# Optimization experiments

Hardware: AMD Instinct MI355X
Metric: run time of the kernel (lower is better)

The kernel has to match this reference:

```python
import jax, jax.numpy as jnp
import numpy as np

B, LC, LQ, H = 64, 1024, 128, 512
NEG = -1e30


def setup_inputs() -> dict:
    key = jax.random.key(0)
    ks = jax.random.split(key, 12)
    s = 1.0 / np.sqrt(H)
    return {
        "c": jax.random.normal(ks[0], (B, LC, H), jnp.float32),
        "q": jax.random.normal(ks[1], (B, LQ, H), jnp.float32),
        "c_mask": jax.random.randint(ks[2], (B, LC), 0, 2, jnp.int32),
        "q_mask": jax.random.randint(ks[3], (B, LQ), 0, 2, jnp.int32),
        "c_weight": jax.random.normal(ks[4], (H, 1), jnp.float32) * s,
        "q_weight": jax.random.normal(ks[5], (H, 1), jnp.float32) * s,
        "cq_weight": jax.random.normal(ks[6], (1, 1, H), jnp.float32) * s,
        "bias": jnp.zeros((1,), jnp.float32),
        "W1": jax.random.normal(ks[7], (H, H), jnp.float32) * s,
        "b1": jnp.zeros((H,), jnp.float32),
        "W2": jax.random.normal(ks[8], (H, H), jnp.float32) * s,
        "b2": jnp.zeros((H,), jnp.float32),
    }


def reference(c, q, c_mask, q_mask, c_weight, q_weight, cq_weight, bias, W1, b1, W2, b2):
    # --- trilinear similarity (BiDAF eq. 1, memory-efficient form) ---
    s0 = c @ c_weight                                   # [B, LC, 1]
    s1 = jnp.swapaxes(q @ q_weight, 1, 2)               # [B, 1, LQ]
    s2 = jnp.einsum('bch,bqh->bcq', c * cq_weight, q)   # [B, LC, LQ]
    sim = s0 + s1 + s2 + bias

    qm = (q_mask != 0)[:, None, :]   # [B, 1, LQ]
    cm = (c_mask != 0)[:, :, None]   # [B, LC, 1]

    # dual masked softmax (dropout is identity in eval mode)
    s1s = jax.nn.softmax(jnp.where(qm, sim, NEG), axis=2)  # c2q weights
    s2s = jax.nn.softmax(jnp.where(cm, sim, NEG), axis=1)  # q2c weights

    a = s1s @ q                                            # [B, LC, H]
    b = jnp.einsum('bcq,bkq->bck', s1s, s2s) @ c           # [B, LC, H]

    # co-attention branch: qprime = relu(lin2(relu(lin1(q))))
    qp = jax.nn.relu(jax.nn.relu(q @ W1 + b1) @ W2 + b2)   # [B, LQ, H]
    scoat = jnp.einsum('bch,bqh->bcq', c, qp)              # [B, LC, LQ]
    sc1 = jax.nn.softmax(jnp.where(qm, scoat, NEG), axis=2)
    sc2 = jax.nn.softmax(jnp.where(cm, scoat, NEG), axis=1)
    acoat = sc1 @ qp                                       # [B, LC, H]
    bcoat = jnp.einsum('bcq,bch->bqh', sc2, c)             # [B, LQ, H]
    scoat3 = sc1 @ bcoat                                   # [B, LC, H]

    return jnp.concatenate([c, a, c * a, c * b, scoat3, acoat], axis=2)  # [B, LC, 6H]
```

## Files before the change

### kernel.cpp

```cpp
#include <hip/hip_runtime.h>
#include <cstdint>
#include <cstddef>

typedef short  bf16x8 __attribute__((ext_vector_type(8)));
typedef float  f32x4  __attribute__((ext_vector_type(4)));

#define NEGV (-1e30f)
#define LDT 40

__device__ __forceinline__ short f2bf(float x){
    union { float f; unsigned u; } v; v.f = x;
    return (short)((v.u + 0x7fffu + ((v.u >> 16) & 1u)) >> 16);
}
__device__ __forceinline__ float bf2f(short h){
    union { float f; unsigned u; } v; v.u = ((unsigned)(unsigned short)h) << 16; return v.f;
}

__global__ __launch_bounds__(256)
void k_prep_w(const float* __restrict__ W1, const float* __restrict__ W2,
              short* __restrict__ W1Th, short* __restrict__ W1Tl,
              short* __restrict__ W2Th, short* __restrict__ W2Tl)
{
    int idx = blockIdx.x * 256 + threadIdx.x;
    int w = idx >> 18;
    int e = idx & ((1 << 18) - 1);
    int n = e & 511, k = e >> 9;
    const float* W = w ? W2 : W1;
    float x = W[k * 512 + n];
    short hi = f2bf(x);
    short lo = f2bf(x - bf2f(hi));
    size_t o = (size_t)n * 512 + k;
    if (w) { W2Th[o] = hi; W2Tl[o] = lo; } else { W1Th[o] = hi; W1Tl[o] = lo; }
}

__global__ __launch_bounds__(256)
void k_transq(const float* __restrict__ q, short* __restrict__ qT)
{
    __shared__ short TT[128 * 136];
    const int t = threadIdx.x;
    const int b = (int)(blockIdx.x >> 2), h0 = (int)(blockIdx.x & 3) * 128;
    #pragma unroll
    for (int it = 0; it < 16; it++) {
        int idx = it * 256 + t;
        int m = idx >> 5, c4 = (idx & 31) * 4;
        float4 v = *(const float4*)(q + ((size_t)b * 128 + m) * 512 + h0 + c4);
        TT[(c4 + 0) * 136 + m] = f2bf(v.x);
        TT[(c4 + 1) * 136 + m] = f2bf(v.y);
        TT[(c4 + 2) * 136 + m] = f2bf(v.z);
        TT[(c4 + 3) * 136 + m] = f2bf(v.w);
    }
    __syncthreads();
    const int h = t >> 1, half = t & 1;
    short* dst = qT + ((size_t)b * 512 + h0 + h) * 128 + half * 64;
    #pragma unroll
    for (int j = 0; j < 8; j++)
        *(bf16x8*)(dst + j * 8) = *(const bf16x8*)&TT[h * 136 + half * 64 + j * 8];
}

template<bool WT>
__global__ __launch_bounds__(256)
void k_linear(const float* __restrict__ X, const short* __restrict__ WTh,
              const short* __restrict__ WTl, const float* __restrict__ bias,
              float* __restrict__ Y, short* __restrict__ YT)
{
    __shared__ short SMEM[4 * 128 * LDT];
    short* Ah = SMEM;
    short* Al = SMEM + 128 * LDT;
    short* Bh = SMEM + 2 * 128 * LDT;
    short* Bl = SMEM + 3 * 128 * LDT;
    const int t = threadIdx.x;
    const int m0 = (int)(blockIdx.x >> 2) * 128;
    const int n0 = (int)(blockIdx.x & 3) * 128;
    const int lane = t & 63;
    const int wr = (t >> 7) & 1, wc = (t >> 6) & 1;
    const int fr = lane & 15, fg = lane >> 4;
    const int srow = t >> 1, sk = (t & 1) * 16;

    f32x4 acc[4][4] = {};

    for (int k0 = 0; k0 < 512; k0 += 32) {
        __syncthreads();
        {
            const float* src = X + (size_t)(m0 + srow) * 512 + k0 + sk;
            float4 f[4];
            #pragma unroll
            for (int i = 0; i < 4; i++) f[i] = ((const float4*)src)[i];
            const float* fv = (const float*)f;
            short hi[16], lo[16];
            #pragma unroll
            for (int j = 0; j < 16; j++) {
                float x = fv[j];
                short h = f2bf(x);
                hi[j] = h; lo[j] = f2bf(x - bf2f(h));
            }
            #pragma unroll
            for (int j = 0; j < 2; j++) {
                *(bf16x8*)&Ah[srow * LDT + sk + j * 8] = *(bf16x8*)&hi[j * 8];
                *(bf16x8*)&Al[srow * LDT + sk + j * 8] = *(bf16x8*)&lo[j * 8];
            }
        }
        {
            const short* sh = WTh + (size_t)(n0 + srow) * 512 + k0 + sk;
            const short* sl = WTl + (size_t)(n0 + srow) * 512 + k0 + sk;
            #pragma unroll
            for (int j = 0; j < 2; j++) {
                *(bf16x8*)&Bh[srow * LDT + sk + j * 8] = ((const bf16x8*)sh)[j];
                *(bf16x8*)&Bl[srow * LDT + sk + j * 8] = ((const bf16x8*)sl)[j];
            }
        }
        __syncthreads();
        bf16x8 a_h[4], a_l[4], b_h[4], b_l[4];
        #pragma unroll
        for (int i = 0; i < 4; i++) {
            int ar = (wr * 64 + i * 16 + fr) * LDT + fg * 8;
            int br = (wc * 64 + i * 16 + fr) * LDT + fg * 8;
            a_h[i] = *(const bf16x8*)&Ah[ar];
            a_l[i] = *(const bf16x8*)&Al[ar];
            b_h[i] = *(const bf16x8*)&Bh[br];
            b_l[i] = *(const bf16x8*)&Bl[br];
        }
        #pragma unroll
        for (int mi = 0; mi < 4; mi++)
        #pragma unroll
        for (int ni = 0; ni < 4; ni++) {
            acc[mi][ni] = __builtin_amdgcn_mfma_f32_16x16x32_bf16(a_h[mi], b_h[ni], acc[mi][ni], 0, 0, 0);
            acc[mi][ni] = __builtin_amdgcn_mfma_f32_16x16x32_bf16(a_h[mi], b_l[ni], acc[mi][ni], 0, 0, 0);
            acc[mi][ni] = __builtin_amdgcn_mfma_f32_16x16x32_bf16(a_l[mi], b_h[ni], acc[mi][ni], 0, 0, 0);
        }
    }
    float bv[4];
    #pragma unroll
    for (int ni = 0; ni < 4; ni++) bv[ni] = bias[n0 + wc * 64 + ni * 16 + fr];
    #pragma unroll
    for (int mi = 0; mi < 4; mi++)
    #pragma unroll
    for (int r = 0; r < 4; r++) {
        int row = m0 + wr * 64 + mi * 16 + fg * 4 + r;
        #pragma unroll
        for (int ni = 0; ni < 4; ni++) {
            float v = fmaxf(acc[mi][ni][r] + bv[ni], 0.f);
            Y[(size_t)row * 512 + n0 + wc * 64 + ni * 16 + fr] = v;
        }
    }
    if (WT) {
        __syncthreads();
        short* TT = SMEM;
        #pragma unroll
        for (int mi = 0; mi < 4; mi++)
        #pragma unroll
        for (int r = 0; r < 4; r++) {
            int ml = wr * 64 + mi * 16 + fg * 4 + r;
            #pragma unroll
            for (int ni = 0; ni < 4; ni++) {
                int nl = wc * 64 + ni * 16 + fr;
                TT[nl * 136 + ml] = f2bf(fmaxf(acc[mi][ni][r] + bv[ni], 0.f));
            }
        }
        __syncthreads();
        const int n = t >> 1, half = t & 1;
        short* dst = YT + ((size_t)(m0 >> 7) * 512 + n0 + n) * 128 + half * 64;
        #pragma unroll
        for (int j = 0; j < 8; j++)
            *(bf16x8*)(dst + j * 8) = *(const bf16x8*)&TT[n * 136 + half * 64 + j * 8];
    }
}

template<bool SPLIT, bool AMUL, bool ADDS>
__global__ __launch_bounds__(256)
void k_att_gemm(const float* __restrict__ Cc, const float* __restrict__ Qq,
                const float* __restrict__ cqw, const float* __restrict__ cwv,
                const float* __restrict__ qwv, const float* __restrict__ biasp,
                const int* __restrict__ qmask, const int* __restrict__ cmask,
                float* __restrict__ Sout, float2* __restrict__ rowst,
                float2* __restrict__ colpart)
{
    __shared__ short Ah[128 * LDT], Bh[128 * LDT];
    __shared__ short Al[SPLIT ? 128 * LDT : 8], Bl[SPLIT ? 128 * LDT : 8];
    __shared__ float cqs[AMUL ? 512 : 8];
    __shared__ float cws[ADDS ? 512 : 8], qws[ADDS ? 512 : 8];
    __shared__ float red[2][128];
    __shared__ float mrowL[128], cmaxL[128];
    __shared__ float s0red[ADDS ? 128 : 1][2], s1red[ADDS ? 128 : 1][2];
    __shared__ float s0arr[ADDS ? 128 : 1], s1arr[ADDS ? 128 : 1];
    __shared__ int qmsL[128], cmsL[128];

    const int t = threadIdx.x;
    const int b  = (int)(blockIdx.x >> 3);
    const int ch = (int)(blockIdx.x & 7);
    const int m0 = ch * 128;
    const int lane = t & 63;
    const int wr = (t >> 7) & 1, wc = (t >> 6) & 1;
    const int fr = lane & 15, fg = lane >> 4;
    const int srow = t >> 1, sk = (t & 1) * 16;

    if (AMUL) { cqs[t] = cqw[t]; cqs[t + 256] = cqw[t + 256]; }
    if (ADDS) {
        cws[t] = cwv[t]; cws[t + 256] = cwv[t + 256];
        qws[t] = qwv[t]; qws[t + 256] = qwv[t + 256];
    }
    if (t < 128) { qmsL[t] = qmask[b * 128 + t]; cmsL[t] = cmask[b * 1024 + m0 + t]; }

    float s0part = 0.f, s1part = 0.f;
    f32x4 acc[4][4] = {};

    for (int k0 = 0; k0 < 512; k0 += 32) {
        __syncthreads();
        {
            const float* src = Cc + ((size_t)b * 1024 + m0 + srow) * 512 + k0 + sk;
            float4 f[4];
            #pragma unroll
            for (int i = 0; i < 4; i++) f[i] = ((const float4*)src)[i];
            const float* fv = (const float*)f;
            short hi[16], lo[16];
            #pragma unroll
            for (int j = 0; j < 16; j++) {
                float raw = fv[j];
                if (ADDS) s0part += raw * cws[k0 + sk + j];
                float x = raw;
                if (AMUL) x *= cqs[k0 + sk + j];
                short h = f2bf(x);
                hi[j] = h;
                if (SPLIT) lo[j] = f2bf(x - bf2f(h));
            }
            #pragma unroll
            for (int j = 0; j < 2; j++) {
                *(bf16x8*)&Ah[srow * LDT + sk + j * 8] = *(bf16x8*)&hi[j * 8];
                if (SPLIT) *(bf16x8*)&Al[srow * LDT + sk + j * 8] = *(bf16x8*)&lo[j * 8];
            }
        }
        {
            const float* src = Qq + ((size_t)b * 128 + srow) * 512 + k0 + sk;
            float4 f[4];
            #pragma unroll
            for (int i = 0; i < 4; i++) f[i] = ((const float4*)src)[i];
            const float* fv = (const float*)f;
            short hi[16], lo[16];
            #pragma unroll
            for (int j = 0; j < 16; j++) {
                float x = fv[j];
                if (ADDS) s1part += x * qws[k0 + sk + j];
                short h = f2bf(x);
                hi[j] = h;
                if (SPLIT) lo[j] = f2bf(x - bf2f(h));
            }
            #pragma unroll
            for (int j = 0; j < 2; j++) {
                *(bf16x8*)&Bh[srow * LDT + sk + j * 8] = *(bf16x8*)&hi[j * 8];
                if (SPLIT) *(bf16x8*)&Bl[srow * LDT + sk + j * 8] = *(bf16x8*)&lo[j * 8];
            }
        }
        __syncthreads();
        bf16x8 a_h[4], b_h[4], a_l[4], b_l[4];
        #pragma unroll
        for (int i = 0; i < 4; i++) {
            int ar = (wr * 64 + i * 16 + fr) * LDT + fg * 8;
            int br = (wc * 64 + i * 16 + fr) * LDT + fg * 8;
            a_h[i] = *(const bf16x8*)&Ah[ar];
            b_h[i] = *(const bf16x8*)&Bh[br];
            if (SPLIT) { a_l[i] = *(const bf16x8*)&Al[ar]; b_l[i] = *(const bf16x8*)&Bl[br]; }
        }
        #pragma unroll
        for (int mi = 0; mi < 4; mi++)
        #pragma unroll
        for (int ni = 0; ni < 4; ni++) {
            acc[mi][ni] = __builtin_amdgcn_mfma_f32_16x16x32_bf16(a_h[mi], b_h[ni], acc[mi][ni], 0, 0, 0);
            if (SPLIT) {
                acc[mi][ni] = __builtin_amdgcn_mfma_f32_16x16x32_bf16(a_h[mi], b_l[ni], acc[mi][ni], 0, 0, 0);
                acc[mi][ni] = __builtin_amdgcn_mfma_f32_16x16x32_bf16(a_l[mi], b_h[ni], acc[mi][ni], 0, 0, 0);
            }
        }
    }

    if (ADDS) { s0red[srow][t & 1] = s0part; s1red[srow][t & 1] = s1part; }
    __syncthreads();
    if (ADDS && t < 128) {
        s0arr[t] = s0red[t][0] + s0red[t][1];
        s1arr[t] = s1red[t][0] + s1red[t][1];
    }
    if (ADDS) __syncthreads();

    if (ADDS) {
        float b0 = biasp[0];
        #pragma unroll
        for (int mi = 0; mi < 4; mi++)
        #pragma unroll
        for (int r = 0; r < 4; r++) {
            float s0r = s0arr[wr * 64 + mi * 16 + fg * 4 + r] + b0;
            #pragma unroll
            for (int ni = 0; ni < 4; ni++)
                acc[mi][ni][r] += s0r + s1arr[wc * 64 + ni * 16 + fr];
        }
    }
    #pragma unroll
    for (int mi = 0; mi < 4; mi++)
    #pragma unroll
    for (int r = 0; r < 4; r++) {
        int row = m0 + wr * 64 + mi * 16 + fg * 4 + r;
        #pragma unroll
        for (int ni = 0; ni < 4; ni++)
            Sout[((size_t)b * 1024 + row) * 128 + wc * 64 + ni * 16 + fr] = acc[mi][ni][r];
    }

    bool qmv[4];
    #pragma unroll
    for (int ni = 0; ni < 4; ni++) qmv[ni] = qmsL[wc * 64 + ni * 16 + fr] != 0;
    bool cmb[4][4];
    #pragma unroll
    for (int mi = 0; mi < 4; mi++)
    #pragma unroll
    for (int r = 0; r < 4; r++) cmb[mi][r] = cmsL[wr * 64 + mi * 16 + fg * 4 + r] != 0;

    float rmax[4][4];
    #pragma unroll
    for (int mi = 0; mi < 4; mi++)
    #pragma unroll
    for (int r = 0; r < 4; r++) {
        float m = NEGV;
        #pragma unroll
        for (int ni = 0; ni < 4; ni++) if (qmv[ni]) m = fmaxf(m, acc[mi][ni][r]);
        #pragma unroll
        for (int off = 1; off < 16; off <<= 1) m = fmaxf(m, __shfl_xor(m, off));
        rmax[mi][r] = m;
    }
    if (fr == 0) {
        #pragma unroll
        for (int mi = 0; mi < 4; mi++)
        #pragma unroll
        for (int r = 0; r < 4; r++) red[wc][wr * 64 + mi * 16 + fg * 4 + r] = rmax[mi][r];
    }
    __syncthreads();
    if (t < 128) mrowL[t] = fmaxf(red[0][t], red[1][t]);
    __syncthreads();
    #pragma unroll
    for (int mi = 0; mi < 4; mi++)
    #pragma unroll
    for (int r = 0; r < 4; r++) {
        float mr = mrowL[wr * 64 + mi * 16 + fg * 4 + r];
        float s = 0.f;
        #pragma unroll
        for (int ni = 0; ni < 4; ni++) if (qmv[ni]) s += __expf(acc[mi][ni][r] - mr);
        #pragma unroll
        for (int off = 1; off < 16; off <<= 1) s += __shfl_xor(s, off);
        if (fr == 0) red[wc][wr * 64 + mi * 16 + fg * 4 + r] = s;
    }
    __syncthreads();
    if (t < 128) rowst[(size_t)b * 1024 + m0 + t] = make_float2(mrowL[t], red[0][t] + red[1][t]);
    __syncthreads();
    float cpart[4];
    #pragma unroll
    for (int ni = 0; ni < 4; ni++) {
        float m = NEGV;
        #pragma unroll
        for (int mi = 0; mi < 4; mi++)
        #pragma unroll
        for (int r = 0; r < 4; r++) if (cmb[mi][r]) m = fmaxf(m, acc[mi][ni][r]);
        m = fmaxf(m, __shfl_xor(m, 16));
        m = fmaxf(m, __shfl_xor(m, 32));
        cpart[ni] = m;
    }
    if (fg == 0) {
        #pragma unroll
        for (int ni = 0; ni < 4; ni++) red[wr][wc * 64 + ni * 16 + fr] = cpart[ni];
    }
    __syncthreads();
    if (t < 128) cmaxL[t] = fmaxf(red[0][t], red[1][t]);
    __syncthreads();
    #pragma unroll
    for (int ni = 0; ni < 4; ni++) {
        float cm = cmaxL[wc * 64 + ni * 16 + fr];
        float s = 0.f;
        #pragma unroll
        for (int mi = 0; mi < 4; mi++)
        #pragma unroll
        for (int r = 0; r < 4; r++) if (cmb[mi][r]) s += __expf(acc[mi][ni][r] - cm);
        s += __shfl_xor(s, 16);
        s += __shfl_xor(s, 32);
        cpart[ni] = s;
    }
    __syncthreads();
    if (fg == 0) {
        #pragma unroll
        for (int ni = 0; ni < 4; ni++) red[wr][wc * 64 + ni * 16 + fr] = cpart[ni];
    }
    __syncthreads();
    if (t < 128) colpart[((size_t)b * 8 + ch) * 128 + t] = make_float2(cmaxL[t], red[0][t] + red[1][t]);
}

__global__ __launch_bounds__(512)
void k_emit(const float* __restrict__ S, const int* __restrict__ qmask,
            const int* __restrict__ cmask, const float2* __restrict__ rowst,
            const float2* __restrict__ colpart, short* __restrict__ Pr,
            short* __restrict__ PcT)
{
    __shared__ float2 colfinL[128];
    const int t = threadIdx.x;
    const int b = (int)(blockIdx.x >> 3), ch = (int)(blockIdx.x & 7);
    const int r0 = ch * 128;
    if (t < 128) {
        float M = NEGV;
        #pragma unroll
        for (int c2 = 0; c2 < 8; c2++) M = fmaxf(M, colpart[((size_t)b * 8 + c2) * 128 + t].x);
        float Ss = 0.f;
        #pragma unroll
        for (int c2 = 0; c2 < 8; c2++) {
            float2 p = colpart[((size_t)b * 8 + c2) * 128 + t];
            Ss += p.y * __expf(p.x - M);
        }
        colfinL[t] = make_float2(M, Ss);
    }
    __syncthreads();
    {
        const int q = t & 127, rg = t >> 7;
        const bool qm = qmask[b * 128 + q] != 0;
        #pragma unroll 8
        for (int i = 0; i < 32; i++) {
            int r = r0 + rg * 32 + i;
            size_t idx = ((size_t)b * 1024 + r) * 128 + q;
            float v = S[idx];
            float2 rs = rowst[(size_t)b * 1024 + r];
            float o = qm ? __expf(v - rs.x) / rs.y : 0.f;
            Pr[idx] = f2bf(o);
        }
    }
    {
        const int q2 = t >> 2, ig = t & 3;
        float2 cs = colfinL[q2];
        float inv = 1.f / cs.y;
        short buf[32];
        #pragma unroll
        for (int i = 0; i < 32; i++) {
            int r = r0 + ig * 32 + i;
            bool cm = cmask[b * 1024 + r] != 0;
            float v = S[((size_t)b * 1024 + r) * 128 + q2];
            buf[i] = f2bf(cm ? __expf(v - cs.x) * inv : 0.f);
        }
        short* dst = PcT + ((size_t)b * 128 + q2) * 1024 + r0 + ig * 32;
        #pragma unroll
        for (int j = 0; j < 4; j++) *(bf16x8*)(dst + j * 8) = *(bf16x8*)&buf[j * 8];
    }
}

__global__ __launch_bounds__(256)
void k_kgemm2(const short* __restrict__ A1, const short* __restrict__ A2,
              const float* __restrict__ Cc, short* __restrict__ Y1T,
              short* __restrict__ Y2T)
{
    __shared__ short Bs[128 * LDT];
    __shared__ short TT[128 * 136];
    const int t = threadIdx.x;
    const int b = (int)(blockIdx.x >> 2);
    const int n0 = (int)(blockIdx.x & 3) * 128;
    const int lane = t & 63;
    const int wr = (t >> 7) & 1, wc = (t >> 6) & 1;
    const int fr = lane & 15, fg = lane >> 4;
    const int n4 = (t & 31) * 4, kk4 = (t >> 5) * 4;
    f32x4 acc1[4][4] = {}, acc2[4][4] = {};
    for (int k0 = 0; k0 < 1024; k0 += 32) {
        __syncthreads();
        {
            const float* bsrc = Cc + ((size_t)b * 1024 + k0 + kk4) * 512 + n0 + n4;
            float4 r0_ = *(const float4*)(bsrc);
            float4 r1_ = *(const float4*)(bsrc + 512);
            float4 r2_ = *(const float4*)(bsrc + 1024);
            float4 r3_ = *(const float4*)(bsrc + 1536);
            const float* p0 = (const float*)&r0_;
            const float* p1 = (const float*)&r1_;
            const float* p2 = (const float*)&r2_;
            const float* p3 = (const float*)&r3_;
            #pragma unroll
            for (int l = 0; l < 4; l++) {
                unsigned d0 = (unsigned)(unsigned short)f2bf(p0[l]) | ((unsigned)(unsigned short)f2bf(p1[l]) << 16);
                unsigned d1 = (unsigned)(unsigned short)f2bf(p2[l]) | ((unsigned)(unsigned short)f2bf(p3[l]) << 16);
                uint2 dd; dd.x = d0; dd.y = d1;
                *(uint2*)&Bs[(n4 + l) * LDT + kk4] = dd;
            }
        }
        __syncthreads();
        bf16x8 a1[4], a2[4], bg[4];
        #pragma unroll
        for (int i = 0; i < 4; i++) {
            size_t arow = (size_t)(b * 128 + wr * 64 + i * 16 + fr) * 1024 + k0 + fg * 8;
            a1[i] = *(const bf16x8*)(A1 + arow);
            a2[i] = *(const bf16x8*)(A2 + arow);
            bg[i] = *(const bf16x8*)&Bs[(wc * 64 + i * 16 + fr) * LDT + fg * 8];
        }
        #pragma unroll
        for (int mi = 0; mi < 4; mi++)
        #pragma unroll
        for (int ni = 0; ni < 4; ni++) {
            acc1[mi][ni] = __builtin_amdgcn_mfma_f32_16x16x32_bf16(a1[mi], bg[ni], acc1[mi][ni], 0, 0, 0);
            acc2[mi][ni] = __builtin_amdgcn_mfma_f32_16x16x32_bf16(a2[mi], bg[ni], acc2[mi][ni], 0, 0, 0);
        }
    }
    const int n = t >> 1, half = t & 1;
    __syncthreads();
    #pragma unroll
    for (int mi = 0; mi < 4; mi++)
    #pragma unroll
    for (int r = 0; r < 4; r++) {
        int ml = wr * 64 + mi * 16 + fg * 4 + r;
        #pragma unroll
        for (int ni = 0; ni < 4; ni++)
            TT[(wc * 64 + ni * 16 + fr) * 136 + ml] = f2bf(acc1[mi][ni][r]);
    }
    __syncthreads();
    {
        short* dst = Y1T + ((size_t)b * 512 + n0 + n) * 128 + half * 64;
        #pragma unroll
        for (int j = 0; j < 8; j++)
            *(bf16x8*)(dst + j * 8) = *(const bf16x8*)&TT[n * 136 + half * 64 + j * 8];
    }
    __syncthreads();
    #pragma unroll
    for (int mi = 0; mi < 4; mi++)
    #pragma unroll
    for (int r = 0; r < 4; r++) {
        int ml = wr * 64 + mi * 16 + fg * 4 + r;
        #pragma unroll
        for (int ni = 0; ni < 4; ni++)
            TT[(wc * 64 + ni * 16 + fr) * 136 + ml] = f2bf(acc2[mi][ni][r]);
    }
    __syncthreads();
    {
        short* dst = Y2T + ((size_t)b * 512 + n0 + n) * 128 + half * 64;
        #pragma unroll
        for (int j = 0; j < 8; j++)
            *(bf16x8*)(dst + j * 8) = *(const bf16x8*)&TT[n * 136 + half * 64 + j * 8];
    }
}

template<bool WITHC>
__global__ __launch_bounds__(256)
void k_epi(const short* __restrict__ Pm, const short* __restrict__ BT1,
           const short* __restrict__ BT2, const float* __restrict__ Cc,
           float* __restrict__ out)
{
    const int t = threadIdx.x;
    const int hb = (int)(blockIdx.x & 3);
    const int mb = (int)((blockIdx.x >> 2) & 7);
    const int b  = (int)(blockIdx.x >> 5);
    const int m0 = mb * 128, h0 = hb * 128;
    const int lane = t & 63;
    const int wr = (t >> 7) & 1, wc = (t >> 6) & 1;
    const int fr = lane & 15, fg = lane >> 4;
    f32x4 acc1[4][4] = {}, acc2[4][4] = {};
    const short* Abase  = Pm  + ((size_t)b * 1024 + m0) * 128;
    const short* B1base = BT1 + ((size_t)b * 512 + h0) * 128;
    const short* B2base = BT2 + ((size_t)b * 512 + h0) * 128;
    #pragma unroll
    for (int kk = 0; kk < 4; kk++) {
        const int k0 = kk * 32;
        bf16x8 af[4], b1[4], b2[4];
        #pragma unroll
        for (int i = 0; i < 4; i++) {
            af[i] = *(const bf16x8*)(Abase  + (size_t)(wr * 64 + i * 16 + fr) * 128 + k0 + fg * 8);
            b1[i] = *(const bf16x8*)(B1base + (size_t)(wc * 64 + i * 16 + fr) * 128 + k0 + fg * 8);
            b2[i] = *(const bf16x8*)(B2base + (size_t)(wc * 64 + i * 16 + fr) * 128 + k0 + fg * 8);
        }
        #pragma unroll
        for (int mi = 0; mi < 4; mi++)
        #pragma unroll
        for (int ni = 0; ni < 4; ni++) {
            acc1[mi][ni] = __builtin_amdgcn_mfma_f32_16x16x32_bf16(af[mi], b1[ni], acc1[mi][ni], 0, 0, 0);
            acc2[mi][ni] = __builtin_amdgcn_mfma_f32_16x16x32_bf16(af[mi], b2[ni], acc2[mi][ni], 0, 0, 0);
        }
    }
    const size_t crow_base = (size_t)b * 1024 + m0;
    #pragma unroll
    for (int mi = 0; mi < 4; mi++)
    #pragma unroll
    for (int r = 0; r < 4; r++) {
        int rowl = wr * 64 + mi * 16 + fg * 4 + r;
        size_t obase = (crow_base + rowl) * 3072 + h0;
        #pragma unroll
        for (int ni = 0; ni < 4; ni++) {
            int col = wc * 64 + ni * 16 + fr;
            float av = acc1[mi][ni][r], bv2 = acc2[mi][ni][r];
            if (WITHC) {
                float cv = Cc[(crow_base + rowl) * 512 + h0 + col];
                out[obase + col]        = cv;
                out[obase + col + 512]  = av;
                out[obase + col + 1024] = cv * av;
                out[obase + col + 1536] = cv * bv2;
            } else {
                out[obase + col + 2048] = bv2;
                out[obase + col + 2560] = av;
            }
        }
    }
}

extern "C" void kernel_launch(void* const* d_in, const int* in_sizes, int n_in,
                              void* d_out, int out_size, void* d_ws, size_t ws_size,
                              hipStream_t stream)
{
    const float* c     = (const float*)d_in[0];
    const float* q     = (const float*)d_in[1];
    const int*   cmask = (const int*)d_in[2];
    const int*   qmask = (const int*)d_in[3];
    const float* cwv   = (const float*)d_in[4];
    const float* qwv   = (const float*)d_in[5];
    const float* cqw   = (const float*)d_in[6];
    const float* bias  = (const float*)d_in[7];
    const float* W1    = (const float*)d_in[8];
    const float* b1    = (const float*)d_in[9];
    const float* W2    = (const float*)d_in[10];
    const float* b2    = (const float*)d_in[11];
    float* out = (float*)d_out;

    char* ws = (char*)d_ws;
    size_t off = 0;
    auto alloc = [&](size_t bytes) -> char* {
        char* p = ws + off;
        off = (off + bytes + 255) & ~(size_t)255;
        return p;
    };
    short* w1th = (short*)alloc(512 * 512 * 2);
    short* w1tl = (short*)alloc(512 * 512 * 2);
    short* w2th = (short*)alloc(512 * 512 * 2);
    short* w2tl = (short*)alloc(512 * 512 * 2);
    float* z1   = (float*)alloc((size_t)8192 * 512 * 4);
    float* qp   = (float*)alloc((size_t)8192 * 512 * 4);
    short* qT   = (short*)alloc((size_t)64 * 512 * 128 * 2);
    short* qpT  = (short*)alloc((size_t)64 * 512 * 128 * 2);
    float* simb = (float*)alloc((size_t)64 * 1024 * 128 * 4);
    float2* rowst   = (float2*)alloc((size_t)64 * 1024 * 8);
    float2* colpart = (float2*)alloc((size_t)64 * 8 * 128 * 8);
    short* s1s  = (short*)alloc((size_t)64 * 1024 * 128 * 2);
    short* s2sT = (short*)alloc((size_t)64 * 128 * 1024 * 2);
    short* sc1  = (short*)alloc((size_t)64 * 1024 * 128 * 2);
    short* sc2T = (short*)alloc((size_t)64 * 128 * 1024 * 2);
    short* binT = (short*)z1;
    short* bcoT = ((short*)z1) + (size_t)64 * 512 * 128;

    k_prep_w<<<2048, 256, 0, stream>>>(W1, W2, w1th, w1tl, w2th, w2tl);
    k_linear<false><<<256, 256, 0, stream>>>(q, w1th, w1tl, b1, z1, nullptr);
    k_linear<true><<<256, 256, 0, stream>>>(z1, w2th, w2tl, b2, qp, qpT);
    k_transq<<<256, 256, 0, stream>>>(q, qT);

    k_att_gemm<false, true, true><<<512, 256, 0, stream>>>(
        c, q, cqw, cwv, qwv, bias, qmask, cmask, simb, rowst, colpart);
    k_emit<<<512, 512, 0, stream>>>(simb, qmask, cmask, rowst, colpart, s1s, s2sT);

    k_att_gemm<true, false, false><<<512, 256, 0, stream>>>(
        c, qp, nullptr, nullptr, nullptr, nullptr, qmask, cmask, simb, rowst, colpart);
    k_emit<<<512, 512, 0, stream>>>(simb, qmask, cmask, rowst, colpart, sc1, sc2T);

    k_kgemm2<<<256, 256, 0, stream>>>(s2sT, sc2T, c, binT, bcoT);

    k_epi<true><<<2048, 256, 0, stream>>>(s1s, qT, binT, c, out);
    k_epi<false><<<2048, 256, 0, stream>>>(sc1, qpT, bcoT, nullptr, out);
}
```

Baseline: 690.7 us.

## Precompute bf16 splits of c and q once and emit row softmax in attention GEMM

Adds prep kernels that convert c into bf16 hi/lo and cq-scaled copies and compute the s0/s1 dot products once, so the attention GEMMs load ready bf16 tiles instead of re-reading and converting fp32 for every block. The row softmax is now finished and written inside the attention GEMM, so the emit kernel only does the column softmax. The k_kgemm2 kernel reads the precomputed bf16 c and double-buffers its shared tile. Block index mapping is changed to interleave batches. The cost is extra workspace and roughly 200MB of additional writes and reads for the c copies.

```diff
diff --git a/kernel.cpp b/kernel.cpp
--- a/kernel.cpp
+++ b/kernel.cpp
@@ -14,6 +14,9 @@
 }
 __device__ __forceinline__ float bf2f(short h){
     union { float f; unsigned u; } v; v.u = ((unsigned)(unsigned short)h) << 16; return v.f;
+}
+__device__ __forceinline__ unsigned packbf(short a, short b){
+    return (unsigned)(unsigned short)a | ((unsigned)(unsigned short)b << 16);
 }
 
 __global__ __launch_bounds__(256)
@@ -34,20 +37,69 @@
 }
 
 __global__ __launch_bounds__(256)
-void k_transq(const float* __restrict__ q, short* __restrict__ qT)
+void k_prep_c(const float* __restrict__ c, const float* __restrict__ cqw,
+              const float* __restrict__ cwv, short* __restrict__ cqc,
+              short* __restrict__ chi, short* __restrict__ clo,
+              float* __restrict__ s0g)
+{
+    __shared__ float cqs[512], cws[512];
+    const int t = threadIdx.x;
+    cqs[t] = cqw[t]; cqs[t + 256] = cqw[t + 256];
+    cws[t] = cwv[t]; cws[t + 256] = cwv[t + 256];
+    __syncthreads();
+    const int R = (int)blockIdx.x * 16 + (t >> 4);
+    const int lane16 = t & 15;
+    const size_t base = (size_t)R * 512;
+    float s0acc = 0.f;
+    #pragma unroll
+    for (int i = 0; i < 8; i++) {
+        int col = lane16 * 4 + i * 64;
+        float4 v = *(const float4*)(c + base + col);
+        short h0 = f2bf(v.x), h1 = f2bf(v.y), h2 = f2bf(v.z), h3 = f2bf(v.w);
+        uint2 dh; dh.x = packbf(h0, h1); dh.y = packbf(h2, h3);
+        *(uint2*)(chi + base + col) = dh;
+        uint2 dl;
+        dl.x = packbf(f2bf(v.x - bf2f(h0)), f2bf(v.y - bf2f(h1)));
+        dl.y = packbf(f2bf(v.z - bf2f(h2)), f2bf(v.w - bf2f(h3)));
+        *(uint2*)(clo + base + col) = dl;
+        uint2 dq;
+        dq.x = packbf(f2bf(v.x * cqs[col]),     f2bf(v.y * cqs[col + 1]));
+        dq.y = packbf(f2bf(v.z * cqs[col + 2]), f2bf(v.w * cqs[col + 3]));
+        *(uint2*)(cqc + base + col) = dq;
+        s0acc += v.x * cws[col] + v.y * cws[col + 1] + v.z * cws[col + 2] + v.w * cws[col + 3];
+    }
+    #pragma unroll
+    for (int off = 1; off < 16; off <<= 1) s0acc += __shfl_xor(s0acc, off);
+    if (lane16 == 0) s0g[R] = s0acc;
+}
+
+__global__ __launch_bounds__(256)
+void k_prep_q(const float* __restrict__ q, const float* __restrict__ qwv,
+              short* __restrict__ q_bf, short* __restrict__ qT,
+              float* __restrict__ s1p)
 {
     __shared__ short TT[128 * 136];
+    __shared__ float qws[128];
     const int t = threadIdx.x;
-    const int b = (int)(blockIdx.x >> 2), h0 = (int)(blockIdx.x & 3) * 128;
+    const int b = (int)(blockIdx.x >> 2), hb = (int)(blockIdx.x & 3), h0 = hb * 128;
+    if (t < 128) qws[t] = qwv[h0 + t];
+    __syncthreads();
     #pragma unroll
     for (int it = 0; it < 16; it++) {
         int idx = it * 256 + t;
         int m = idx >> 5, c4 = (idx & 31) * 4;
         float4 v = *(const float4*)(q + ((size_t)b * 128 + m) * 512 + h0 + c4);
-        TT[(c4 + 0) * 136 + m] = f2bf(v.x);
-        TT[(c4 + 1) * 136 + m] = f2bf(v.y);
-        TT[(c4 + 2) * 136 + m] = f2bf(v.z);
-        TT[(c4 + 3) * 136 + m] = f2bf(v.w);
+        short h0s = f2bf(v.x), h1s = f2bf(v.y), h2s = f2bf(v.z), h3s = f2bf(v.w);
+        TT[(c4 + 0) * 136 + m] = h0s;
+        TT[(c4 + 1) * 136 + m] = h1s;
+        TT[(c4 + 2) * 136 + m] = h2s;
+        TT[(c4 + 3) * 136 + m] = h3s;
+        uint2 d; d.x = packbf(h0s, h1s); d.y = packbf(h2s, h3s);
+        *(uint2*)(q_bf + ((size_t)b * 128 + m) * 512 + h0 + c4) = d;
+        float dot = v.x * qws[c4] + v.y * qws[c4 + 1] + v.z * qws[c4 + 2] + v.w * qws[c4 + 3];
+        #pragma unroll
+        for (int off = 1; off < 32; off <<= 1) dot += __shfl_xor(dot, off);
+        if ((t & 31) == 0) s1p[((size_t)b * 4 + hb) * 128 + m] = dot;
     }
     __syncthreads();
     const int h = t >> 1, half = t & 1;
@@ -61,7 +113,8 @@
 __global__ __launch_bounds__(256)
 void k_linear(const float* __restrict__ X, const short* __restrict__ WTh,
               const short* __restrict__ WTl, const float* __restrict__ bias,
-              float* __restrict__ Y, short* __restrict__ YT)
+              float* __restrict__ Y, short* __restrict__ Yh,
+              short* __restrict__ Yl, short* __restrict__ YT)
 {
     __shared__ short SMEM[4 * 128 * LDT];
     short* Ah = SMEM;
@@ -131,18 +184,33 @@
     float bv[4];
     #pragma unroll
     for (int ni = 0; ni < 4; ni++) bv[ni] = bias[n0 + wc * 64 + ni * 16 + fr];
-    #pragma unroll
-    for (int mi = 0; mi < 4; mi++)
-    #pragma unroll
-    for (int r = 0; r < 4; r++) {
-        int row = m0 + wr * 64 + mi * 16 + fg * 4 + r;
-        #pragma unroll
-        for (int ni = 0; ni < 4; ni++) {
-            float v = fmaxf(acc[mi][ni][r] + bv[ni], 0.f);
-            Y[(size_t)row * 512 + n0 + wc * 64 + ni * 16 + fr] = v;
-        }
-    }
-    if (WT) {
+
+    if (!WT) {
+        #pragma unroll
+        for (int mi = 0; mi < 4; mi++)
+        #pragma unroll
+        for (int r = 0; r < 4; r++) {
+            int row = m0 + wr * 64 + mi * 16 + fg * 4 + r;
+            #pragma unroll
+            for (int ni = 0; ni < 4; ni++)
+                Y[(size_t)row * 512 + n0 + wc * 64 + ni * 16 + fr] =
+                    fmaxf(acc[mi][ni][r] + bv[ni], 0.f);
+        }
+    } else {
+        #pragma unroll
+        for (int mi = 0; mi < 4; mi++)
+        #pragma unroll
+        for (int r = 0; r < 4; r++) {
+            int row = m0 + wr * 64 + mi * 16 + fg * 4 + r;
+            #pragma unroll
+            for (int ni = 0; ni < 4; ni++) {
+                float v = fmaxf(acc[mi][ni][r] + bv[ni], 0.f);
+                short h = f2bf(v);
+                size_t o = (size_t)row * 512 + n0 + wc * 64 + ni * 16 + fr;
+                Yh[o] = h;
+                Yl[o] = f2bf(v - bf2f(h));
+            }
+        }
         __syncthreads();
         short* TT = SMEM;
         #pragma unroll
@@ -151,10 +219,9 @@
         for (int r = 0; r < 4; r++) {
             int ml = wr * 64 + mi * 16 + fg * 4 + r;
             #pragma unroll
-            for (int ni = 0; ni < 4; ni++) {
-                int nl = wc * 64 + ni * 16 + fr;
-                TT[nl * 136 + ml] = f2bf(fmaxf(acc[mi][ni][r] + bv[ni], 0.f));
-            }
+            for (int ni = 0; ni < 4; ni++)
+                TT[(wc * 64 + ni * 16 + fr) * 136 + ml] =
+                    f2bf(fmaxf(acc[mi][ni][r] + bv[ni], 0.f));
         }
         __syncthreads();
         const int n = t >> 1, half = t & 1;
@@ -165,89 +232,56 @@
     }
 }
 
-template<bool SPLIT, bool AMUL, bool ADDS>
+template<bool SPLIT, bool ADDS>
 __global__ __launch_bounds__(256)
-void k_att_gemm(const float* __restrict__ Cc, const float* __restrict__ Qq,
-                const float* __restrict__ cqw, const float* __restrict__ cwv,
-                const float* __restrict__ qwv, const float* __restrict__ biasp,
-                const int* __restrict__ qmask, const int* __restrict__ cmask,
-                float* __restrict__ Sout, float2* __restrict__ rowst,
-                float2* __restrict__ colpart)
+void k_att(const short* __restrict__ Ahg, const short* __restrict__ Alg,
+           const short* __restrict__ Bhg, const short* __restrict__ Blg,
+           const float* __restrict__ s0g, const float* __restrict__ s1pg,
+           const float* __restrict__ biasp, const int* __restrict__ qmask,
+           const int* __restrict__ cmask, float* __restrict__ simb,
+           short* __restrict__ Pr, float2* __restrict__ colpart)
 {
     __shared__ short Ah[128 * LDT], Bh[128 * LDT];
     __shared__ short Al[SPLIT ? 128 * LDT : 8], Bl[SPLIT ? 128 * LDT : 8];
-    __shared__ float cqs[AMUL ? 512 : 8];
-    __shared__ float cws[ADDS ? 512 : 8], qws[ADDS ? 512 : 8];
     __shared__ float red[2][128];
-    __shared__ float mrowL[128], cmaxL[128];
-    __shared__ float s0red[ADDS ? 128 : 1][2], s1red[ADDS ? 128 : 1][2];
-    __shared__ float s0arr[ADDS ? 128 : 1], s1arr[ADDS ? 128 : 1];
+    __shared__ float mrowL[128], rinvL[128], cmaxL[128];
+    __shared__ float s0L[ADDS ? 128 : 1], s1L[ADDS ? 128 : 1];
     __shared__ int qmsL[128], cmsL[128];
 
     const int t = threadIdx.x;
-    const int b  = (int)(blockIdx.x >> 3);
-    const int ch = (int)(blockIdx.x & 7);
+    const int b  = (int)(blockIdx.x & 63);
+    const int ch = (int)(blockIdx.x >> 6);
     const int m0 = ch * 128;
     const int lane = t & 63;
     const int wr = (t >> 7) & 1, wc = (t >> 6) & 1;
     const int fr = lane & 15, fg = lane >> 4;
     const int srow = t >> 1, sk = (t & 1) * 16;
 
-    if (AMUL) { cqs[t] = cqw[t]; cqs[t + 256] = cqw[t + 256]; }
-    if (ADDS) {
-        cws[t] = cwv[t]; cws[t + 256] = cwv[t + 256];
-        qws[t] = qwv[t]; qws[t + 256] = qwv[t + 256];
-    }
-    if (t < 128) { qmsL[t] = qmask[b * 128 + t]; cmsL[t] = cmask[b * 1024 + m0 + t]; }
-
-    float s0part = 0.f, s1part = 0.f;
+    if (t < 128) {
+        qmsL[t] = qmask[b * 128 + t];
+        cmsL[t] = cmask[b * 1024 + m0 + t];
+        if (ADDS) {
+            s0L[t] = s0g[b * 1024 + m0 + t];
+            s1L[t] = s1pg[((size_t)b * 4 + 0) * 128 + t] + s1pg[((size_t)b * 4 + 1) * 128 + t]
+                   + s1pg[((size_t)b * 4 + 2) * 128 + t] + s1pg[((size_t)b * 4 + 3) * 128 + t];
+        }
+    }
+
+    const size_t aoff = ((size_t)b * 1024 + m0 + srow) * 512;
+    const size_t boff = ((size_t)b * 128 + srow) * 512;
     f32x4 acc[4][4] = {};
 
     for (int k0 = 0; k0 < 512; k0 += 32) {
         __syncthreads();
-        {
-            const float* src = Cc + ((size_t)b * 1024 + m0 + srow) * 512 + k0 + sk;
-            float4 f[4];
-            #pragma unroll
-            for (int i = 0; i < 4; i++) f[i] = ((const float4*)src)[i];
-            const float* fv = (const float*)f;
-            short hi[16], lo[16];
-            #pragma unroll
-            for (int j = 0; j < 16; j++) {
-                float raw = fv[j];
-                if (ADDS) s0part += raw * cws[k0 + sk + j];
-                float x = raw;
-                if (AMUL) x *= cqs[k0 + sk + j];
-                short h = f2bf(x);
-                hi[j] = h;
-                if (SPLIT) lo[j] = f2bf(x - bf2f(h));
-            }
-            #pragma unroll
-            for (int j = 0; j < 2; j++) {
-                *(bf16x8*)&Ah[srow * LDT + sk + j * 8] = *(bf16x8*)&hi[j * 8];
-                if (SPLIT) *(bf16x8*)&Al[srow * LDT + sk + j * 8] = *(bf16x8*)&lo[j * 8];
-            }
-        }
-        {
-            const float* src = Qq + ((size_t)b * 128 + srow) * 512 + k0 + sk;
-            float4 f[4];
-            #pragma unroll
-            for (int i = 0; i < 4; i++) f[i] = ((const float4*)src)[i];
-            const float* fv = (const float*)f;
-            short hi[16], lo[16];
-            #pragma unroll
-            for (int j = 0; j < 16; j++) {
-                float x = fv[j];
-                if (ADDS) s1part += x * qws[k0 + sk + j];
-                short h = f2bf(x);
-                hi[j] = h;
-                if (SPLIT) lo[j] = f2bf(x - bf2f(h));
-            }
-            #pragma unroll
-            for (int j = 0; j < 2; j++) {
-                *(bf16x8*)&Bh[srow * LDT + sk + j * 8] = *(bf16x8*)&hi[j * 8];
-                if (SPLIT) *(bf16x8*)&Bl[srow * LDT + sk + j * 8] = *(bf16x8*)&lo[j * 8];
-            }
+        *(uint4*)&Ah[srow * LDT + sk]     = *(const uint4*)(Ahg + aoff + k0 + sk);
+        *(uint4*)&Ah[srow * LDT + sk + 8] = *(const uint4*)(Ahg + aoff + k0 + sk + 8);
+        *(uint4*)&Bh[srow * LDT + sk]     = *(const uint4*)(Bhg + boff + k0 + sk);
+        *(uint4*)&Bh[srow * LDT + sk + 8] = *(const uint4*)(Bhg + boff + k0 + sk + 8);
+        if (SPLIT) {
+            *(uint4*)&Al[srow * LDT + sk]     = *(const uint4*)(Alg + aoff + k0 + sk);
+            *(uint4*)&Al[srow * LDT + sk + 8] = *(const uint4*)(Alg + aoff + k0 + sk + 8);
+            *(uint4*)&Bl[srow * LDT + sk]     = *(const uint4*)(Blg + boff + k0 + sk);
+            *(uint4*)&Bl[srow * LDT + sk + 8] = *(const uint4*)(Blg + boff + k0 + sk + 8);
         }
         __syncthreads();
         bf16x8 a_h[4], b_h[4], a_l[4], b_l[4];
@@ -271,24 +305,16 @@
         }
     }
 
-    if (ADDS) { s0red[srow][t & 1] = s0part; s1red[srow][t & 1] = s1part; }
-    __syncthreads();
-    if (ADDS && t < 128) {
-        s0arr[t] = s0red[t][0] + s0red[t][1];
-        s1arr[t] = s1red[t][0] + s1red[t][1];
-    }
-    if (ADDS) __syncthreads();
-
     if (ADDS) {
         float b0 = biasp[0];
         #pragma unroll
         for (int mi = 0; mi < 4; mi++)
         #pragma unroll
         for (int r = 0; r < 4; r++) {
-            float s0r = s0arr[wr * 64 + mi * 16 + fg * 4 + r] + b0;
+            float s0r = s0L[wr * 64 + mi * 16 + fg * 4 + r] + b0;
             #pragma unroll
             for (int ni = 0; ni < 4; ni++)
-                acc[mi][ni][r] += s0r + s1arr[wc * 64 + ni * 16 + fr];
+                acc[mi][ni][r] += s0r + s1L[wc * 64 + ni * 16 + fr];
         }
     }
     #pragma unroll
@@ -298,7 +324,7 @@
         int row = m0 + wr * 64 + mi * 16 + fg * 4 + r;
         #pragma unroll
         for (int ni = 0; ni < 4; ni++)
-            Sout[((size_t)b * 1024 + row) * 128 + wc * 64 + ni * 16 + fr] = acc[mi][ni][r];
+            simb[((size_t)b * 1024 + row) * 128 + wc * 64 + ni * 16 + fr] = acc[mi][ni][r];
     }
 
     bool qmv[4];
@@ -310,7 +336,6 @@
     #pragma unroll
     for (int r = 0; r < 4; r++) cmb[mi][r] = cmsL[wr * 64 + mi * 16 + fg * 4 + r] != 0;
 
-    float rmax[4][4];
     #pragma unroll
     for (int mi = 0; mi < 4; mi++)
     #pragma unroll
@@ -320,13 +345,7 @@
         for (int ni = 0; ni < 4; ni++) if (qmv[ni]) m = fmaxf(m, acc[mi][ni][r]);
         #pragma unroll
         for (int off = 1; off < 16; off <<= 1) m = fmaxf(m, __shfl_xor(m, off));
-        rmax[mi][r] = m;
-    }
-    if (fr == 0) {
-        #pragma unroll
-        for (int mi = 0; mi < 4; mi++)
-        #pragma unroll
-        for (int r = 0; r < 4; r++) red[wc][wr * 64 + mi * 16 + fg * 4 + r] = rmax[mi][r];
+        if (fr == 0) red[wc][wr * 64 + mi * 16 + fg * 4 + r] = m;
     }
     __syncthreads();
     if (t < 128) mrowL[t] = fmaxf(red[0][t], red[1][t]);
@@ -344,8 +363,21 @@
         if (fr == 0) red[wc][wr * 64 + mi * 16 + fg * 4 + r] = s;
     }
     __syncthreads();
-    if (t < 128) rowst[(size_t)b * 1024 + m0 + t] = make_float2(mrowL[t], red[0][t] + red[1][t]);
-    __syncthreads();
+    if (t < 128) rinvL[t] = 1.f / (red[0][t] + red[1][t]);
+    __syncthreads();
+    #pragma unroll
+    for (int mi = 0; mi < 4; mi++)
+    #pragma unroll
+    for (int r = 0; r < 4; r++) {
+        int rowl = wr * 64 + mi * 16 + fg * 4 + r;
+        float mr = mrowL[rowl], iv = rinvL[rowl];
+        size_t obase = ((size_t)b * 1024 + m0 + rowl) * 128;
+        #pragma unroll
+        for (int ni = 0; ni < 4; ni++) {
+            float o = qmv[ni] ? __expf(acc[mi][ni][r] - mr) * iv : 0.f;
+            Pr[obase + wc * 64 + ni * 16 + fr] = f2bf(o);
+        }
+    }
     float cpart[4];
     #pragma unroll
     for (int ni = 0; ni < 4; ni++) {
@@ -387,10 +419,8 @@
 }
 
 __global__ __launch_bounds__(512)
-void k_emit(const float* __restrict__ S, const int* __restrict__ qmask,
-            const int* __restrict__ cmask, const float2* __restrict__ rowst,
-            const float2* __restrict__ colpart, short* __restrict__ Pr,
-            short* __restrict__ PcT)
+void k_emit2(const float* __restrict__ S, const int* __restrict__ cmask,
+             const float2* __restrict__ colpart, short* __restrict__ PcT)
 {
     __shared__ float2 colfinL[128];
     const int t = threadIdx.x;
@@ -409,80 +439,77 @@
         colfinL[t] = make_float2(M, Ss);
     }
     __syncthreads();
-    {
-        const int q = t & 127, rg = t >> 7;
-        const bool qm = qmask[b * 128 + q] != 0;
-        #pragma unroll 8
-        for (int i = 0; i < 32; i++) {
-            int r = r0 + rg * 32 + i;
-            size_t idx = ((size_t)b * 1024 + r) * 128 + q;
-            float v = S[idx];
-            float2 rs = rowst[(size_t)b * 1024 + r];
-            float o = qm ? __expf(v - rs.x) / rs.y : 0.f;
-            Pr[idx] = f2bf(o);
-        }
-    }
-    {
-        const int q2 = t >> 2, ig = t & 3;
-        float2 cs = colfinL[q2];
-        float inv = 1.f / cs.y;
-        short buf[32];
-        #pragma unroll
-        for (int i = 0; i < 32; i++) {
-            int r = r0 + ig * 32 + i;
-            bool cm = cmask[b * 1024 + r] != 0;
-            float v = S[((size_t)b * 1024 + r) * 128 + q2];
-            buf[i] = f2bf(cm ? __expf(v - cs.x) * inv : 0.f);
-        }
-        short* dst = PcT + ((size_t)b * 128 + q2) * 1024 + r0 + ig * 32;
-        #pragma unroll
-        for (int j = 0; j < 4; j++) *(bf16x8*)(dst + j * 8) = *(bf16x8*)&buf[j * 8];
-    }
+    const int q2 = t >> 2, ig = t & 3;
+    float2 cs = colfinL[q2];
+    float inv = 1.f / cs.y;
+    short buf[32];
+    #pragma unroll
+    for (int i = 0; i < 32; i++) {
+        int r = r0 + ig * 32 + i;
+        bool cm = cmask[b * 1024 + r] != 0;
+        float v = S[((size_t)b * 1024 + r) * 128 + q2];
+        buf[i] = f2bf(cm ? __expf(v - cs.x) * inv : 0.f);
+    }
+    short* dst = PcT + ((size_t)b * 128 + q2) * 1024 + r0 + ig * 32;
+    #pragma unroll
+    for (int j = 0; j < 4; j++) *(bf16x8*)(dst + j * 8) = *(bf16x8*)&buf[j * 8];
 }
 
 __global__ __launch_bounds__(256)
 void k_kgemm2(const short* __restrict__ A1, const short* __restrict__ A2,
-              const float* __restrict__ Cc, short* __restrict__ Y1T,
+              const short* __restrict__ Chi, short* __restrict__ Y1T,
               short* __restrict__ Y2T)
 {
-    __shared__ short Bs[128 * LDT];
+    __shared__ short Bs[2][128 * LDT];
     __shared__ short TT[128 * 136];
     const int t = threadIdx.x;
-    const int b = (int)(blockIdx.x >> 2);
-    const int n0 = (int)(blockIdx.x & 3) * 128;
+    const int b  = (int)(blockIdx.x & 63);
+    const int n0 = (int)(blockIdx.x >> 6) * 128;
     const int lane = t & 63;
     const int wr = (t >> 7) & 1, wc = (t >> 6) & 1;
     const int fr = lane & 15, fg = lane >> 4;
-    const int n4 = (t & 31) * 4, kk4 = (t >> 5) * 4;
+    const int n4 = (t & 31) * 4, kp2 = (t >> 5) * 2;
+
     f32x4 acc1[4][4] = {}, acc2[4][4] = {};
+
+    auto load_e = [&](int k0, uint2* e) {
+        #pragma unroll
+        for (int s = 0; s < 2; s++) {
+            const short* p = Chi + ((size_t)b * 1024 + k0 + kp2 + s * 16) * 512 + n0 + n4;
+            e[s * 2]     = *(const uint2*)(p);
+            e[s * 2 + 1] = *(const uint2*)(p + 512);
+        }
+    };
+    auto store_b = [&](const uint2* e, int buf) {
+        #pragma unroll
+        for (int s = 0; s < 2; s++) {
+            const short* r0p = (const short*)&e[s * 2];
+            const short* r1p = (const short*)&e[s * 2 + 1];
+            #pragma unroll
+            for (int l = 0; l < 4; l++)
+                *(unsigned*)&Bs[buf][(n4 + l) * LDT + kp2 + s * 16] = packbf(r0p[l], r1p[l]);
+        }
+    };
+
+    {
+        uint2 e[4];
+        load_e(0, e);
+        store_b(e, 0);
+    }
+    __syncthreads();
+
     for (int k0 = 0; k0 < 1024; k0 += 32) {
-        __syncthreads();
-        {
-            const float* bsrc = Cc + ((size_t)b * 1024 + k0 + kk4) * 512 + n0 + n4;
-            float4 r0_ = *(const float4*)(bsrc);
-            float4 r1_ = *(const float4*)(bsrc + 512);
-            float4 r2_ = *(const float4*)(bsrc + 1024);
-            float4 r3_ = *(const float4*)(bsrc + 1536);
-            const float* p0 = (const float*)&r0_;
-            const float* p1 = (const float*)&r1_;
-            const float* p2 = (const float*)&r2_;
-            const float* p3 = (const float*)&r3_;
-            #pragma unroll
-            for (int l = 0; l < 4; l++) {
-                unsigned d0 = (unsigned)(unsigned short)f2bf(p0[l]) | ((unsigned)(unsigned short)f2bf(p1[l]) << 16);
-                unsigned d1 = (unsigned)(unsigned short)f2bf(p2[l]) | ((unsigned)(unsigned short)f2bf(p3[l]) << 16);
-                uint2 dd; dd.x = d0; dd.y = d1;
-                *(uint2*)&Bs[(n4 + l) * LDT + kk4] = dd;
-            }
-        }
-        __syncthreads();
+        const int cur = (k0 >> 5) & 1;
+        const bool more = (k0 + 32) < 1024;
+        uint2 e[4];
+        if (more) load_e(k0 + 32, e);
         bf16x8 a1[4], a2[4], bg[4];
         #pragma unroll
         for (int i = 0; i < 4; i++) {
             size_t arow = (size_t)(b * 128 + wr * 64 + i * 16 + fr) * 1024 + k0 + fg * 8;
             a1[i] = *(const bf16x8*)(A1 + arow);
             a2[i] = *(const bf16x8*)(A2 + arow);
-            bg[i] = *(const bf16x8*)&Bs[(wc * 64 + i * 16 + fr) * LDT + fg * 8];
+            bg[i] = *(const bf16x8*)&Bs[cur][(wc * 64 + i * 16 + fr) * LDT + fg * 8];
         }
         #pragma unroll
         for (int mi = 0; mi < 4; mi++)
@@ -491,9 +518,11 @@
             acc1[mi][ni] = __builtin_amdgcn_mfma_f32_16x16x32_bf16(a1[mi], bg[ni], acc1[mi][ni], 0, 0, 0);
             acc2[mi][ni] = __builtin_amdgcn_mfma_f32_16x16x32_bf16(a2[mi], bg[ni], acc2[mi][ni], 0, 0, 0);
         }
-    }
+        if (more) store_b(e, cur ^ 1);
+        __syncthreads();
+    }
+
     const int n = t >> 1, half = t & 1;
-    __syncthreads();
     #pragma unroll
     for (int mi = 0; mi < 4; mi++)
     #pragma unroll
@@ -619,12 +648,18 @@
     short* w1tl = (short*)alloc(512 * 512 * 2);
     short* w2th = (short*)alloc(512 * 512 * 2);
     short* w2tl = (short*)alloc(512 * 512 * 2);
+    short* cqc  = (short*)alloc((size_t)64 * 1024 * 512 * 2);
+    short* chi  = (short*)alloc((size_t)64 * 1024 * 512 * 2);
+    short* clo  = (short*)alloc((size_t)64 * 1024 * 512 * 2);
+    float* s0g  = (float*)alloc(64 * 1024 * 4);
+    float* s1p  = (float*)alloc(64 * 4 * 128 * 4);
+    short* q_bf = (short*)alloc((size_t)64 * 128 * 512 * 2);
+    short* qT   = (short*)alloc((size_t)64 * 512 * 128 * 2);
     float* z1   = (float*)alloc((size_t)8192 * 512 * 4);
-    float* qp   = (float*)alloc((size_t)8192 * 512 * 4);
-    short* qT   = (short*)alloc((size_t)64 * 512 * 128 * 2);
+    short* qp_h = (short*)alloc((size_t)8192 * 512 * 2);
+    short* qp_l = (short*)alloc((size_t)8192 * 512 * 2);
     short* qpT  = (short*)alloc((size_t)64 * 512 * 128 * 2);
     float* simb = (float*)alloc((size_t)64 * 1024 * 128 * 4);
-    float2* rowst   = (float2*)alloc((size_t)64 * 1024 * 8);
     float2* colpart = (float2*)alloc((size_t)64 * 8 * 128 * 8);
     short* s1s  = (short*)alloc((size_t)64 * 1024 * 128 * 2);
     short* s2sT = (short*)alloc((size_t)64 * 128 * 1024 * 2);
@@ -634,19 +669,20 @@
     short* bcoT = ((short*)z1) + (size_t)64 * 512 * 128;
 
     k_prep_w<<<2048, 256, 0, stream>>>(W1, W2, w1th, w1tl, w2th, w2tl);
-    k_linear<false><<<256, 256, 0, stream>>>(q, w1th, w1tl, b1, z1, nullptr);
-    k_linear<true><<<256, 256, 0, stream>>>(z1, w2th, w2tl, b2, qp, qpT);
-    k_transq<<<256, 256, 0, stream>>>(q, qT);
-
-    k_att_gemm<false, true, true><<<512, 256, 0, stream>>>(
-        c, q, cqw, cwv, qwv, bias, qmask, cmask, simb, rowst, colpart);
-    k_emit<<<512, 512, 0, stream>>>(simb, qmask, cmask, rowst, colpart, s1s, s2sT);
-
-    k_att_gemm<true, false, false><<<512, 256, 0, stream>>>(
-        c, qp, nullptr, nullptr, nullptr, nullptr, qmask, cmask, simb, rowst, colpart);
-    k_emit<<<512, 512, 0, stream>>>(simb, qmask, cmask, rowst, colpart, sc1, sc2T);
-
-    k_kgemm2<<<256, 256, 0, stream>>>(s2sT, sc2T, c, binT, bcoT);
+    k_prep_c<<<4096, 256, 0, stream>>>(c, cqw, cwv, cqc, chi, clo, s0g);
+    k_prep_q<<<256, 256, 0, stream>>>(q, qwv, q_bf, qT, s1p);
+    k_linear<false><<<256, 256, 0, stream>>>(q, w1th, w1tl, b1, z1, nullptr, nullptr, nullptr);
+    k_linear<true><<<256, 256, 0, stream>>>(z1, w2th, w2tl, b2, nullptr, qp_h, qp_l, qpT);
+
+    k_att<false, true><<<512, 256, 0, stream>>>(
+        cqc, nullptr, q_bf, nullptr, s0g, s1p, bias, qmask, cmask, simb, s1s, colpart);
+    k_emit2<<<512, 512, 0, stream>>>(simb, cmask, colpart, s2sT);
+
+    k_att<true, false><<<512, 256, 0, stream>>>(
+        chi, clo, qp_h, qp_l, nullptr, nullptr, nullptr, qmask, cmask, simb, sc1, colpart);
+    k_emit2<<<512, 512, 0, stream>>>(simb, cmask, colpart, sc2T);
+
+    k_kgemm2<<<256, 256, 0, stream>>>(s2sT, sc2T, chi, binT, bcoT);
 
     k_epi<true><<<2048, 256, 0, stream>>>(s1s, qT, binT, c, out);
     k_epi<false><<<2048, 256, 0, stream>>>(sc1, qpT, bcoT, nullptr, out);
```

After: 738.5 us. 6.9% more time.
